# Performance work log

Hardware: AMD Instinct MI355X
Metric: run time of the kernel (lower is better)

The kernel has to match this reference:

```python
import jax, jax.numpy as jnp
import numpy as np

B, T, D = 1, 4096, 1024
H, KD, VD = 16, 64, 64
MIN_THETA, MAX_THETA = 1.0, 10000.0


def setup_inputs() -> dict:
    key = jax.random.key(0)
    k0, k1, k2 = jax.random.split(key, 3)
    x = jax.random.normal(k0, (B, T, D), dtype=jnp.float32)
    W_in = jax.random.normal(k1, ((2 * KD + VD) * H, D), dtype=jnp.float32) * 0.02
    b_in = jnp.zeros(((2 * KD + VD) * H,), dtype=jnp.float32)
    W_out = jax.random.normal(k2, (D, H * VD), dtype=jnp.float32) * 0.02
    b_out = jnp.zeros((D,), dtype=jnp.float32)
    return {"x": x, "W_in": W_in, "b_in": b_in, "W_out": W_out, "b_out": b_out}


def _sin_cos(t, d, dtype):
    # geometric sequence of thetas over half the head dim
    half = d // 2
    p = jnp.arange(half, dtype=dtype) / (half - 1)
    thetas = MIN_THETA * (MAX_THETA / MIN_THETA) ** p  # [half]
    pos = jnp.arange(t, dtype=dtype)[:, None] / thetas[None, :]  # [T, half]
    return jnp.sin(pos), jnp.cos(pos)


def _rope(x, sin, cos):
    d = x.shape[-1] // 2
    x_hi, x_lo = x[..., :d], x[..., d:]
    y_lo = x_lo * cos + x_hi * sin
    y_hi = x_hi * cos - x_lo * sin
    return jnp.concatenate([y_lo, y_hi], axis=-1)


def reference(x, W_in, b_in, W_out, b_out):
    b, t, _ = x.shape
    proj = x @ W_in.T + b_in  # [B, T, (2KD+VD)*H]
    i1, i2 = KD * H, 2 * KD * H
    q = proj[..., :i1].reshape(b, t, H, KD).transpose(0, 2, 1, 3)   # [B,H,T,KD]
    k = proj[..., i1:i2].reshape(b, t, H, KD).transpose(0, 2, 1, 3)
    v = proj[..., i2:].reshape(b, t, H, VD).transpose(0, 2, 1, 3)   # [B,H,T,VD]
    sin, cos = _sin_cos(t, KD, x.dtype)
    q = _rope(q, sin, cos)
    k = _rope(k, sin, cos)
    scale = 1.0 / np.sqrt(KD)
    att = jnp.einsum('bhqd,bhkd->bhqk', q, k) * jnp.asarray(scale, x.dtype)
    mask = jnp.tril(jnp.ones((t, t), dtype=bool))  # causal
    att = jnp.where(mask[None, None], att, jnp.asarray(-jnp.inf, x.dtype))
    att = jax.nn.softmax(att, axis=-1)
    y = jnp.einsum('bhqk,bhkd->bhqd', att, v)
    y = y.transpose(0, 2, 1, 3).reshape(b, t, H * VD)
    return y @ W_out.T + b_out
```

## Files before the change

### kernel.cpp

```cpp
#include <hip/hip_runtime.h>
#include <math.h>

#define T_SEQ 4096
#define DMODEL 1024
#define NH 16
#define HD 64
#define NQT (T_SEQ / 64)

typedef _Float16 f16x4 __attribute__((ext_vector_type(4)));
typedef _Float16 f16x8 __attribute__((ext_vector_type(8)));
typedef float f32x4 __attribute__((ext_vector_type(4)));

#define HTD ((size_t)NH * T_SEQ * HD)
#define PREC 68

__global__ __launch_bounds__(256)
void sincos_table_kernel(float* __restrict__ tab) {
    int idx = blockIdx.x * 256 + threadIdx.x;
    if (idx >= T_SEQ * 32) return;
    int t = idx >> 5, j = idx & 31;
    double p = (double)((float)j / 31.0f);
    float theta = (float)pow(10000.0, p);
    float ang = (float)t / theta;
    double a = (double)ang;
    tab[t * 64 + j]      = (float)sin(a);
    tab[t * 64 + 32 + j] = (float)cos(a);
}

__global__ __launch_bounds__(256)
void cast3_kernel(const float* __restrict__ x, const float* __restrict__ wi,
                  const float* __restrict__ wo, _Float16* __restrict__ x16,
                  _Float16* __restrict__ wi16, _Float16* __restrict__ wo16) {
    size_t gid = (size_t)blockIdx.x * 256 + threadIdx.x;
    const float* src; _Float16* dst; size_t i;
    if (gid < 524288)       { src = x;  dst = x16;  i = gid; }
    else if (gid < 917504)  { src = wi; dst = wi16; i = gid - 524288; }
    else                    { src = wo; dst = wo16; i = gid - 917504; }
    float4 a = *((const float4*)src + i * 2);
    float4 b = *((const float4*)src + i * 2 + 1);
    f16x8 o = {(_Float16)a.x, (_Float16)a.y, (_Float16)a.z, (_Float16)a.w,
               (_Float16)b.x, (_Float16)b.y, (_Float16)b.z, (_Float16)b.w};
    *((f16x8*)dst + i) = o;
}

__global__ __launch_bounds__(256)
void rope16_kernel(_Float16* __restrict__ q16, _Float16* __restrict__ k16,
                   const float* __restrict__ tab) {
    int idx = blockIdx.x * 256 + threadIdx.x;
    int j = idx & 31;
    int t = (idx >> 5) & (T_SEQ - 1);
    int h = (idx >> 17) & (NH - 1);
    int z = idx >> 21;
    float s = tab[t * 64 + j];
    float c = tab[t * 64 + 32 + j];
    _Float16* base = (z ? k16 : q16) + ((size_t)h * T_SEQ + t) * HD;
    float a = (float)base[j], b = (float)base[j + 32];
    float lo = b * c + a * s;
    float hi = a * c - b * s;
    if (z == 0) { lo *= 0.18033688f; hi *= 0.18033688f; }
    base[j]      = (_Float16)lo;
    base[j + 32] = (_Float16)hi;
}

template<int EPI>
__global__ __launch_bounds__(256)
void gemm16_kernel(const _Float16* __restrict__ A, const _Float16* __restrict__ B,
                   const float* __restrict__ bias, float* __restrict__ out,
                   _Float16* __restrict__ outv, int M, int N, int K, int gx) {
    __shared__ _Float16 Alds[128 * 64];
    __shared__ _Float16 Blds[128 * 64];
    const int tid = threadIdx.x;
    const int w = tid >> 6, lane = tid & 63, lq = lane & 15, lg = lane >> 4;
    const int wr = w >> 1, wc = w & 1;

    int cpx = (int)gridDim.x >> 3;
    int tileid = (blockIdx.x & 7) * cpx + (blockIdx.x >> 3);
    const int bx = tileid % gx, by = tileid / gx;
    const int row0 = by * 128, col0 = bx * 128;

    const int ra = tid >> 1, ha = tid & 1;
    const _Float16* Ap = A + (size_t)(row0 + ra) * K + ha * 32;
    const _Float16* Bp = B + (size_t)(col0 + ra) * K + ha * 32;
    char* Awr = (char*)Alds + ra * 128;
    char* Bwr = (char*)Blds + ra * 128;
    int wsw[4];
#pragma unroll
    for (int j = 0; j < 4; ++j) wsw[j] = ((ha * 4 + j) ^ (ra & 7)) * 16;

    f32x4 acc[4][4] = {};
    f16x8 sa[4], sb[4];
#pragma unroll
    for (int j = 0; j < 4; ++j) {
        sa[j] = *(const f16x8*)(Ap + j * 8);
        sb[j] = *(const f16x8*)(Bp + j * 8);
    }

    const int nkt = K >> 6;
    for (int kt = 0; kt < nkt; ++kt) {
        __syncthreads();
#pragma unroll
        for (int j = 0; j < 4; ++j) {
            *(f16x8*)(Awr + wsw[j]) = sa[j];
            *(f16x8*)(Bwr + wsw[j]) = sb[j];
        }
        __syncthreads();
        if (kt + 1 < nkt) {
            int kn = (kt + 1) << 6;
#pragma unroll
            for (int j = 0; j < 4; ++j) {
                sa[j] = *(const f16x8*)(Ap + kn + j * 8);
                sb[j] = *(const f16x8*)(Bp + kn + j * 8);
            }
        }
#pragma unroll
        for (int ks = 0; ks < 2; ++ks) {
            f16x8 af[4], bf[4];
            const int cofs = ((ks * 4 + lg) ^ (lq & 7)) * 16;
#pragma unroll
            for (int i = 0; i < 4; ++i) {
                int rA = wr * 64 + i * 16 + lq;
                int rB = wc * 64 + i * 16 + lq;
                af[i] = *(const f16x8*)((char*)Alds + rA * 128 + cofs);
                bf[i] = *(const f16x8*)((char*)Blds + rB * 128 + cofs);
            }
#pragma unroll
            for (int mi = 0; mi < 4; ++mi)
#pragma unroll
                for (int nj = 0; nj < 4; ++nj)
                    acc[mi][nj] = __builtin_amdgcn_mfma_f32_16x16x32_f16(
                        af[mi], bf[nj], acc[mi][nj], 0, 0, 0);
        }
    }

    if (EPI == 0) {
#pragma unroll
        for (int nj = 0; nj < 4; ++nj) {
            int n = col0 + wc * 64 + nj * 16 + lq;
            float bv = bias[n];
#pragma unroll
            for (int mi = 0; mi < 4; ++mi) {
                int t0 = row0 + wr * 64 + mi * 16 + lg * 4;
#pragma unroll
                for (int r = 0; r < 4; ++r)
                    out[(size_t)(t0 + r) * N + n] = acc[mi][nj][r] + bv;
            }
        }
    } else {
        const int tensor = col0 >> 10;
        const int m0b = row0 + wr * 64;
        if (tensor == 2) {
#pragma unroll
            for (int nj = 0; nj < 4; ++nj) {
                int n = col0 + wc * 64 + nj * 16 + lq;
                int nn = n & 1023; int hh = nn >> 6, d = nn & 63;
                float bv = bias[n];
                _Float16* dv = outv + 2 * HTD + (size_t)(hh * 64 + d) * T_SEQ;
#pragma unroll
                for (int mi = 0; mi < 4; ++mi) {
                    int t0 = m0b + mi * 16 + lg * 4;
                    f16x4 val = {(_Float16)(acc[mi][nj][0] + bv),
                                 (_Float16)(acc[mi][nj][1] + bv),
                                 (_Float16)(acc[mi][nj][2] + bv),
                                 (_Float16)(acc[mi][nj][3] + bv)};
                    *(f16x4*)(dv + t0) = val;
                }
            }
        } else {
            _Float16* dst = outv + (size_t)tensor * HTD;
#pragma unroll
            for (int nj = 0; nj < 4; ++nj) {
                int n = col0 + wc * 64 + nj * 16 + lq;
                int nn = n & 1023; int hh = nn >> 6, d = nn & 63;
                float bv = bias[n];
                _Float16* dcol = dst + (size_t)hh * T_SEQ * HD + d;
#pragma unroll
                for (int mi = 0; mi < 4; ++mi) {
                    int t0 = m0b + mi * 16 + lg * 4;
#pragma unroll
                    for (int r = 0; r < 4; ++r)
                        dcol[(size_t)(t0 + r) * HD] = (_Float16)(acc[mi][nj][r] + bv);
                }
            }
        }
    }
}

__device__ __forceinline__ void softmax_step(f32x4 s[4], float& m, float& lp,
                                             f32x4 acc[4], _Float16* Pw,
                                             int lq, int lg) {
    float tmax = s[0][0];
#pragma unroll
    for (int mb = 0; mb < 4; ++mb)
#pragma unroll
        for (int r = 0; r < 4; ++r) tmax = fmaxf(tmax, s[mb][r]);
    if (__ballot(tmax > m + 11.5f)) {
        float g = fmaxf(tmax, __shfl_xor(tmax, 16));
        g = fmaxf(g, __shfl_xor(g, 32));
        float mn  = fmaxf(m, g);
        float scl = exp2f(m - mn);
        m = mn;
        lp *= scl;
#pragma unroll
        for (int mb = 0; mb < 4; ++mb)
#pragma unroll
            for (int r = 0; r < 4; ++r) acc[mb][r] *= scl;
    }
    float tsum = 0.f;
#pragma unroll
    for (int mb = 0; mb < 4; ++mb) {
        float p0 = exp2f(s[mb][0] - m), p1 = exp2f(s[mb][1] - m);
        float p2 = exp2f(s[mb][2] - m), p3 = exp2f(s[mb][3] - m);
        tsum += (p0 + p1) + (p2 + p3);
        f16x4 pk = {(_Float16)p0, (_Float16)p1, (_Float16)p2, (_Float16)p3};
        *(f16x4*)(Pw + (mb * 2 + (lg >> 1)) * 128 + lq * 8 + (lg & 1) * 4) = pk;
    }
    lp += tsum;
}

__global__ __launch_bounds__(256)
void attn_kernel(const _Float16* __restrict__ q16, const _Float16* __restrict__ k16,
                 const _Float16* __restrict__ v16t, float* __restrict__ part) {
    __shared__ _Float16 Klds[2][64 * 64];
    __shared__ _Float16 Vlds[2][64 * 64];
    __shared__ _Float16 Plds[4 * 16 * 64];

    const int tid  = threadIdx.x;
    const int w    = tid >> 6;
    const int lane = tid & 63;
    const int lq   = lane & 15;
    const int lg   = lane >> 4;

    const int bid   = blockIdx.x;
    const int h     = ((bid & 7) << 1) | ((bid >> 3) & 1);
    const int rest  = bid >> 4;
    const int qt    = (NQT - 1) - (rest >> 1);
    const int chunk = rest & 1;
    const int nkt   = qt + 1;
    const int half0 = (nkt + 1) >> 1;
    const int c0    = chunk ? half0 : 0;
    const int c1    = chunk ? nkt   : half0;

    const _Float16* qh = q16  + (size_t)h * T_SEQ * HD;
    const _Float16* kh = k16  + (size_t)h * T_SEQ * HD;
    const _Float16* vh = v16t + (size_t)h * HD * T_SEQ;

    const int qrow = qt * 64 + w * 16 + lq;

    f16x8 qf[2];
    qf[0] = *(const f16x8*)(qh + (size_t)qrow * HD + lg * 8);
    qf[1] = *(const f16x8*)(qh + (size_t)qrow * HD + lg * 8 + 32);

    const int srow = tid >> 4;
    const int scol = (tid & 15) * 4;
    const int schk = (tid & 15) >> 1;
    const int ssub = (tid & 1) * 8;

    _Float16* Pw = Plds + w * 1024;

    float m_r = -3e38f, lp = 0.f;
    f32x4 acc[4] = {};

    if (c0 < c1) {
        f16x4 kreg[4], vreg[4];
#pragma unroll
        for (int it = 0; it < 4; ++it) {
            int row = srow + it * 16;
            kreg[it] = *(const f16x4*)(kh + (size_t)(c0 * 64 + row) * HD + scol);
            vreg[it] = *(const f16x4*)(vh + (size_t)row * T_SEQ + c0 * 64 + scol);
        }
#pragma unroll
        for (int it = 0; it < 4; ++it) {
            int row = srow + it * 16;
            int chk = schk ^ (row & 7);
            *(f16x4*)((char*)Klds[0] + row * 128 + chk * 16 + ssub) = kreg[it];
            *(f16x4*)((char*)Vlds[0] + row * 128 + chk * 16 + ssub) = vreg[it];
        }

        int cur = 0;
        for (int kt = c0; kt < c1; ++kt) {
            __syncthreads();
            if (kt + 1 < c1) {
                const int k0n = (kt + 1) * 64;
#pragma unroll
                for (int it = 0; it < 4; ++it) {
                    int row = srow + it * 16;
                    kreg[it] = *(const f16x4*)(kh + (size_t)(k0n + row) * HD + scol);
                    vreg[it] = *(const f16x4*)(vh + (size_t)row * T_SEQ + k0n + scol);
                }
            }

            f32x4 s[4] = {};
            __builtin_amdgcn_s_setprio(1);
#pragma unroll
            for (int mb = 0; mb < 4; ++mb) {
                int row = mb * 16 + lq;
#pragma unroll
                for (int ks = 0; ks < 2; ++ks) {
                    f16x8 kf = *(const f16x8*)((char*)Klds[cur] + row * 128 +
                                               (((lg + 4 * ks) ^ (lq & 7)) * 16));
                    s[mb] = __builtin_amdgcn_mfma_f32_16x16x32_f16(kf, qf[ks], s[mb], 0, 0, 0);
                }
            }
            __builtin_amdgcn_s_setprio(0);
            if (kt == qt) {
                const int qloc = w * 16 + lq;
#pragma unroll
                for (int mb = 0; mb < 4; ++mb)
#pragma unroll
                    for (int r = 0; r < 4; ++r)
                        if (mb * 16 + lg * 4 + r > qloc) s[mb][r] = -3e38f;
            }

            softmax_step(s, m_r, lp, acc, Pw, lq, lg);

            f16x8 pf[2];
            pf[0] = *(const f16x8*)(Pw + lg * 128 + lq * 8);
            pf[1] = *(const f16x8*)(Pw + (lg + 4) * 128 + lq * 8);
            __builtin_amdgcn_s_setprio(1);
#pragma unroll
            for (int mb = 0; mb < 4; ++mb) {
                int row = mb * 16 + lq;
#pragma unroll
                for (int ks = 0; ks < 2; ++ks) {
                    f16x8 vf = *(const f16x8*)((char*)Vlds[cur] + row * 128 +
                                               (((lg + 4 * ks) ^ (lq & 7)) * 16));
                    acc[mb] = __builtin_amdgcn_mfma_f32_16x16x32_f16(vf, pf[ks], acc[mb], 0, 0, 0);
                }
            }
            __builtin_amdgcn_s_setprio(0);

            if (kt + 1 < c1) {
#pragma unroll
                for (int it = 0; it < 4; ++it) {
                    int row = srow + it * 16;
                    int chk = schk ^ (row & 7);
                    *(f16x4*)((char*)Klds[cur ^ 1] + row * 128 + chk * 16 + ssub) = kreg[it];
                    *(f16x4*)((char*)Vlds[cur ^ 1] + row * 128 + chk * 16 + ssub) = vreg[it];
                }
                cur ^= 1;
            }
        }
    }

    float lsum = lp + __shfl_xor(lp, 16); lsum += __shfl_xor(lsum, 32);
    float* rec = part + ((size_t)((h * NQT + qt) * 2 + chunk) * 64 + w * 16 + lq) * PREC;
#pragma unroll
    for (int mb = 0; mb < 4; ++mb)
        *(float4*)(rec + mb * 16 + lg * 4) =
            make_float4(acc[mb][0], acc[mb][1], acc[mb][2], acc[mb][3]);
    if (lg == 0) { rec[64] = m_r; rec[65] = lsum; }
}

__global__ __launch_bounds__(256)
void combine_kernel(const float* __restrict__ part, _Float16* __restrict__ y16) {
    const int bid = blockIdx.x;
    const int h = bid >> 6, qt = bid & 63;
    const int r  = threadIdx.x >> 2;
    const int dq = (threadIdx.x & 3) * 16;

    const float* r0 = part + ((size_t)((h * NQT + qt) * 2 + 0) * 64 + r) * PREC;
    const float* r1 = part + ((size_t)((h * NQT + qt) * 2 + 1) * 64 + r) * PREC;
    float m0 = r0[64], l0 = r0[65];
    float m1 = r1[64], l1 = r1[65];
    float mx = fmaxf(m0, m1);
    float w0 = exp2f(m0 - mx), w1 = exp2f(m1 - mx);
    float inv = 1.f / (l0 * w0 + l1 * w1);
    w0 *= inv; w1 *= inv;

    const int qrow = qt * 64 + r;
    _Float16* yp = y16 + (size_t)qrow * DMODEL + h * HD + dq;
#pragma unroll
    for (int j = 0; j < 2; ++j) {
        float4 a0 = *(const float4*)(r0 + dq + j * 8);
        float4 b0 = *(const float4*)(r0 + dq + j * 8 + 4);
        float4 a1 = *(const float4*)(r1 + dq + j * 8);
        float4 b1 = *(const float4*)(r1 + dq + j * 8 + 4);
        f16x8 o = {(_Float16)(a0.x * w0 + a1.x * w1), (_Float16)(a0.y * w0 + a1.y * w1),
                   (_Float16)(a0.z * w0 + a1.z * w1), (_Float16)(a0.w * w0 + a1.w * w1),
                   (_Float16)(b0.x * w0 + b1.x * w1), (_Float16)(b0.y * w0 + b1.y * w1),
                   (_Float16)(b0.z * w0 + b1.z * w1), (_Float16)(b0.w * w0 + b1.w * w1)};
        *(f16x8*)(yp + j * 8) = o;
    }
}

extern "C" void kernel_launch(void* const* d_in, const int* in_sizes, int n_in,
                              void* d_out, int out_size, void* d_ws, size_t ws_size,
                              hipStream_t stream) {
    const float* x     = (const float*)d_in[0];
    const float* W_in  = (const float*)d_in[1];
    const float* b_in  = (const float*)d_in[2];
    const float* W_out = (const float*)d_in[3];
    const float* b_out = (const float*)d_in[4];
    float* out = (float*)d_out;

    float* ws = (float*)d_ws;
    float* tab = ws;
    _Float16* fb   = (_Float16*)(ws + (size_t)T_SEQ * 64);
    _Float16* q16  = fb;
    _Float16* k16  = fb + HTD;
    _Float16* v16t = fb + 2 * HTD;
    _Float16* x16  = fb + 3 * HTD;
    _Float16* y16  = x16;
    _Float16* wi16 = x16 + (size_t)T_SEQ * DMODEL;
    _Float16* wo16 = wi16 + (size_t)3072 * DMODEL;
    float* part = (float*)(wo16 + (size_t)DMODEL * DMODEL);

    sincos_table_kernel<<<(T_SEQ * 32 + 255) / 256, 256, 0, stream>>>(tab);
    cast3_kernel<<<4096, 256, 0, stream>>>(x, W_in, W_out, x16, wi16, wo16);

    gemm16_kernel<1><<<768, 256, 0, stream>>>(
        x16, wi16, b_in, nullptr, q16, T_SEQ, 3072, DMODEL, 24);

    rope16_kernel<<<(2 * NH * T_SEQ * 32) / 256, 256, 0, stream>>>(q16, k16, tab);

    attn_kernel<<<2048, 256, 0, stream>>>(q16, k16, v16t, part);

    combine_kernel<<<NH * NQT, 256, 0, stream>>>(part, y16);

    gemm16_kernel<0><<<256, 256, 0, stream>>>(
        y16, wo16, b_out, out, nullptr, T_SEQ, DMODEL, DMODEL, 8);
}
```

Baseline: 233.3 us.

## Fuse RoPE into QKV GEMM epilogue, merge prep kernels, MFMA row sums

Merges the sincos table and cast kernels into a single prep launch. RoPE and the Q scale are now applied in the QKV GEMM epilogue, so the separate rope pass that re-read and re-wrote Q and K is gone. The attention kernel computes the softmax row sum with an MFMA against a ones vector instead of scalar adds and shuffles. Costs are extra table loads in the GEMM epilogue, still-scattered scalar stores, and the row sum now accumulates the fp16-rounded probabilities.

```diff
diff --git a/kernel.cpp b/kernel.cpp
--- a/kernel.cpp
+++ b/kernel.cpp
@@ -15,58 +15,39 @@
 #define PREC 68
 
 __global__ __launch_bounds__(256)
-void sincos_table_kernel(float* __restrict__ tab) {
-    int idx = blockIdx.x * 256 + threadIdx.x;
-    if (idx >= T_SEQ * 32) return;
-    int t = idx >> 5, j = idx & 31;
-    double p = (double)((float)j / 31.0f);
-    float theta = (float)pow(10000.0, p);
-    float ang = (float)t / theta;
-    double a = (double)ang;
-    tab[t * 64 + j]      = (float)sin(a);
-    tab[t * 64 + 32 + j] = (float)cos(a);
-}
-
-__global__ __launch_bounds__(256)
-void cast3_kernel(const float* __restrict__ x, const float* __restrict__ wi,
-                  const float* __restrict__ wo, _Float16* __restrict__ x16,
-                  _Float16* __restrict__ wi16, _Float16* __restrict__ wo16) {
-    size_t gid = (size_t)blockIdx.x * 256 + threadIdx.x;
-    const float* src; _Float16* dst; size_t i;
-    if (gid < 524288)       { src = x;  dst = x16;  i = gid; }
-    else if (gid < 917504)  { src = wi; dst = wi16; i = gid - 524288; }
-    else                    { src = wo; dst = wo16; i = gid - 917504; }
-    float4 a = *((const float4*)src + i * 2);
-    float4 b = *((const float4*)src + i * 2 + 1);
-    f16x8 o = {(_Float16)a.x, (_Float16)a.y, (_Float16)a.z, (_Float16)a.w,
-               (_Float16)b.x, (_Float16)b.y, (_Float16)b.z, (_Float16)b.w};
-    *((f16x8*)dst + i) = o;
-}
-
-__global__ __launch_bounds__(256)
-void rope16_kernel(_Float16* __restrict__ q16, _Float16* __restrict__ k16,
-                   const float* __restrict__ tab) {
-    int idx = blockIdx.x * 256 + threadIdx.x;
-    int j = idx & 31;
-    int t = (idx >> 5) & (T_SEQ - 1);
-    int h = (idx >> 17) & (NH - 1);
-    int z = idx >> 21;
-    float s = tab[t * 64 + j];
-    float c = tab[t * 64 + 32 + j];
-    _Float16* base = (z ? k16 : q16) + ((size_t)h * T_SEQ + t) * HD;
-    float a = (float)base[j], b = (float)base[j + 32];
-    float lo = b * c + a * s;
-    float hi = a * c - b * s;
-    if (z == 0) { lo *= 0.18033688f; hi *= 0.18033688f; }
-    base[j]      = (_Float16)lo;
-    base[j + 32] = (_Float16)hi;
+void prep_kernel(const float* __restrict__ x, const float* __restrict__ wi,
+                 const float* __restrict__ wo, _Float16* __restrict__ x16,
+                 _Float16* __restrict__ wi16, _Float16* __restrict__ wo16,
+                 float* __restrict__ tab) {
+    if (blockIdx.x < 4096) {
+        size_t gid = (size_t)blockIdx.x * 256 + threadIdx.x;
+        const float* src; _Float16* dst; size_t i;
+        if (gid < 524288)       { src = x;  dst = x16;  i = gid; }
+        else if (gid < 917504)  { src = wi; dst = wi16; i = gid - 524288; }
+        else                    { src = wo; dst = wo16; i = gid - 917504; }
+        float4 a = *((const float4*)src + i * 2);
+        float4 b = *((const float4*)src + i * 2 + 1);
+        f16x8 o = {(_Float16)a.x, (_Float16)a.y, (_Float16)a.z, (_Float16)a.w,
+                   (_Float16)b.x, (_Float16)b.y, (_Float16)b.z, (_Float16)b.w};
+        *((f16x8*)dst + i) = o;
+    } else {
+        int idx = (int)(blockIdx.x - 4096) * 256 + threadIdx.x;
+        int t = idx >> 5, j = idx & 31;
+        double p = (double)((float)j / 31.0f);
+        float theta = (float)pow(10000.0, p);
+        float ang = (float)t / theta;
+        double a = (double)ang;
+        tab[t * 64 + j]      = (float)sin(a);
+        tab[t * 64 + 32 + j] = (float)cos(a);
+    }
 }
 
 template<int EPI>
 __global__ __launch_bounds__(256)
 void gemm16_kernel(const _Float16* __restrict__ A, const _Float16* __restrict__ B,
                    const float* __restrict__ bias, float* __restrict__ out,
-                   _Float16* __restrict__ outv, int M, int N, int K, int gx) {
+                   _Float16* __restrict__ outv, const float* __restrict__ tab,
+                   int M, int N, int K, int gx) {
     __shared__ _Float16 Alds[128 * 64];
     __shared__ _Float16 Blds[128 * 64];
     const int tid = threadIdx.x;
@@ -166,28 +147,36 @@
                 }
             }
         } else {
-            _Float16* dst = outv + (size_t)tensor * HTD;
-#pragma unroll
-            for (int nj = 0; nj < 4; ++nj) {
-                int n = col0 + wc * 64 + nj * 16 + lq;
-                int nn = n & 1023; int hh = nn >> 6, d = nn & 63;
-                float bv = bias[n];
-                _Float16* dcol = dst + (size_t)hh * T_SEQ * HD + d;
-#pragma unroll
-                for (int mi = 0; mi < 4; ++mi) {
-                    int t0 = m0b + mi * 16 + lg * 4;
-#pragma unroll
-                    for (int r = 0; r < 4; ++r)
-                        dcol[(size_t)(t0 + r) * HD] = (_Float16)(acc[mi][nj][r] + bv);
-                }
-            }
-        }
-    }
-}
-
-__device__ __forceinline__ void softmax_step(f32x4 s[4], float& m, float& lp,
-                                             f32x4 acc[4], _Float16* Pw,
-                                             int lq, int lg) {
+            const float qs = (tensor == 0) ? 0.18033688f : 1.0f;
+            const int hh = ((col0 & 1023) >> 6) + wc;
+            _Float16* dcol = outv + (size_t)tensor * HTD + (size_t)hh * T_SEQ * HD;
+            const int nb = col0 + wc * 64 + lq;
+            float blo[2] = {bias[nb], bias[nb + 16]};
+            float bhi[2] = {bias[nb + 32], bias[nb + 48]};
+#pragma unroll
+            for (int mi = 0; mi < 4; ++mi) {
+#pragma unroll
+                for (int r = 0; r < 4; ++r) {
+                    int t = m0b + mi * 16 + lg * 4 + r;
+                    const float* tb = tab + t * 64;
+#pragma unroll
+                    for (int nj = 0; nj < 2; ++nj) {
+                        int j = nj * 16 + lq;
+                        float sn = tb[j], cs = tb[32 + j];
+                        float a = acc[mi][nj][r] + blo[nj];
+                        float b = acc[mi][nj + 2][r] + bhi[nj];
+                        dcol[(size_t)t * HD + j]      = (_Float16)((b * cs + a * sn) * qs);
+                        dcol[(size_t)t * HD + j + 32] = (_Float16)((a * cs - b * sn) * qs);
+                    }
+                }
+            }
+        }
+    }
+}
+
+__device__ __forceinline__ void softmax_step(f32x4 s[4], float& m,
+                                             f32x4 acc[4], f32x4& lacc,
+                                             _Float16* Pw, int lq, int lg) {
     float tmax = s[0][0];
 #pragma unroll
     for (int mb = 0; mb < 4; ++mb)
@@ -199,22 +188,19 @@
         float mn  = fmaxf(m, g);
         float scl = exp2f(m - mn);
         m = mn;
-        lp *= scl;
+#pragma unroll
+        for (int r = 0; r < 4; ++r) lacc[r] *= scl;
 #pragma unroll
         for (int mb = 0; mb < 4; ++mb)
 #pragma unroll
             for (int r = 0; r < 4; ++r) acc[mb][r] *= scl;
     }
-    float tsum = 0.f;
 #pragma unroll
     for (int mb = 0; mb < 4; ++mb) {
-        float p0 = exp2f(s[mb][0] - m), p1 = exp2f(s[mb][1] - m);
-        float p2 = exp2f(s[mb][2] - m), p3 = exp2f(s[mb][3] - m);
-        tsum += (p0 + p1) + (p2 + p3);
-        f16x4 pk = {(_Float16)p0, (_Float16)p1, (_Float16)p2, (_Float16)p3};
+        f16x4 pk = {(_Float16)exp2f(s[mb][0] - m), (_Float16)exp2f(s[mb][1] - m),
+                    (_Float16)exp2f(s[mb][2] - m), (_Float16)exp2f(s[mb][3] - m)};
         *(f16x4*)(Pw + (mb * 2 + (lg >> 1)) * 128 + lq * 8 + (lg & 1) * 4) = pk;
     }
-    lp += tsum;
 }
 
 __global__ __launch_bounds__(256)
@@ -250,6 +236,9 @@
     qf[0] = *(const f16x8*)(qh + (size_t)qrow * HD + lg * 8);
     qf[1] = *(const f16x8*)(qh + (size_t)qrow * HD + lg * 8 + 32);
 
+    const f16x8 ones = {(_Float16)1, (_Float16)1, (_Float16)1, (_Float16)1,
+                        (_Float16)1, (_Float16)1, (_Float16)1, (_Float16)1};
+
     const int srow = tid >> 4;
     const int scol = (tid & 15) * 4;
     const int schk = (tid & 15) >> 1;
@@ -257,8 +246,9 @@
 
     _Float16* Pw = Plds + w * 1024;
 
-    float m_r = -3e38f, lp = 0.f;
+    float m_r = -3e38f;
     f32x4 acc[4] = {};
+    f32x4 lacc = {};
 
     if (c0 < c1) {
         f16x4 kreg[4], vreg[4];
@@ -311,12 +301,14 @@
                         if (mb * 16 + lg * 4 + r > qloc) s[mb][r] = -3e38f;
             }
 
-            softmax_step(s, m_r, lp, acc, Pw, lq, lg);
+            softmax_step(s, m_r, acc, lacc, Pw, lq, lg);
 
             f16x8 pf[2];
             pf[0] = *(const f16x8*)(Pw + lg * 128 + lq * 8);
             pf[1] = *(const f16x8*)(Pw + (lg + 4) * 128 + lq * 8);
             __builtin_amdgcn_s_setprio(1);
+            lacc = __builtin_amdgcn_mfma_f32_16x16x32_f16(ones, pf[0], lacc, 0, 0, 0);
+            lacc = __builtin_amdgcn_mfma_f32_16x16x32_f16(ones, pf[1], lacc, 0, 0, 0);
 #pragma unroll
             for (int mb = 0; mb < 4; ++mb) {
                 int row = mb * 16 + lq;
@@ -342,13 +334,12 @@
         }
     }
 
-    float lsum = lp + __shfl_xor(lp, 16); lsum += __shfl_xor(lsum, 32);
     float* rec = part + ((size_t)((h * NQT + qt) * 2 + chunk) * 64 + w * 16 + lq) * PREC;
 #pragma unroll
     for (int mb = 0; mb < 4; ++mb)
         *(float4*)(rec + mb * 16 + lg * 4) =
             make_float4(acc[mb][0], acc[mb][1], acc[mb][2], acc[mb][3]);
-    if (lg == 0) { rec[64] = m_r; rec[65] = lsum; }
+    if (lg == 0) { rec[64] = m_r; rec[65] = lacc[0]; }
 }
 
 __global__ __launch_bounds__(256)
@@ -405,18 +396,15 @@
     _Float16* wo16 = wi16 + (size_t)3072 * DMODEL;
     float* part = (float*)(wo16 + (size_t)DMODEL * DMODEL);
 
-    sincos_table_kernel<<<(T_SEQ * 32 + 255) / 256, 256, 0, stream>>>(tab);
-    cast3_kernel<<<4096, 256, 0, stream>>>(x, W_in, W_out, x16, wi16, wo16);
+    prep_kernel<<<4608, 256, 0, stream>>>(x, W_in, W_out, x16, wi16, wo16, tab);
 
     gemm16_kernel<1><<<768, 256, 0, stream>>>(
-        x16, wi16, b_in, nullptr, q16, T_SEQ, 3072, DMODEL, 24);
-
-    rope16_kernel<<<(2 * NH * T_SEQ * 32) / 256, 256, 0, stream>>>(q16, k16, tab);
+        x16, wi16, b_in, nullptr, q16, tab, T_SEQ, 3072, DMODEL, 24);
 
     attn_kernel<<<2048, 256, 0, stream>>>(q16, k16, v16t, part);
 
     combine_kernel<<<NH * NQT, 256, 0, stream>>>(part, y16);
 
     gemm16_kernel<0><<<256, 256, 0, stream>>>(
-        y16, wo16, b_out, out, nullptr, T_SEQ, DMODEL, DMODEL, 8);
-}
+        y16, wo16, b_out, out, nullptr, nullptr, T_SEQ, DMODEL, DMODEL, 8);
+}
```

Measured after the change: 226.7 us. 2.8% less time.
